# Kernel optimization log

Hardware: AMD Instinct MI355X
Metric: run time of the kernel (lower is better)

Reference implementation:

```python
import jax, jax.numpy as jnp
import numpy as np

N, M, D = 16384, 4096, 512
GAMMA = 1.0


def setup_inputs() -> dict:
    key = jax.random.key(0)
    kx, kc = jax.random.split(key)
    x = jax.random.normal(kx, (N, D), dtype=jnp.float32)
    centroids = jax.random.normal(kc, (M, D), dtype=jnp.float32)
    return {"x": x, "centroids": centroids}


def reference(x, centroids):
    x_sq = jnp.sum(x * x, axis=-1, keepdims=True)            # [N, 1]
    c_sq = jnp.sum(centroids * centroids, axis=-1)           # [M]
    cross = jnp.einsum('nd,md->nm', x, centroids)            # [N, M]
    dist_sq = x_sq + c_sq[None, :] - 2.0 * cross
    dist_sq = jnp.maximum(dist_sq, 0.0)  # clamp tiny negatives from fp error
    return jnp.exp(-GAMMA * dist_sq)
```

## Files before the change

kernel.cpp:

```cpp
#include <hip/hip_runtime.h>
#include <hip/hip_bf16.h>


#define NN 16384
#define MM 4096
#define DD 512

typedef float f32x4 __attribute__((ext_vector_type(4)));
typedef long i64x2 __attribute__((ext_vector_type(2)));

__device__ __forceinline__ void async16(const void* g, void* l) {
  __builtin_amdgcn_global_load_lds(
      (const __attribute__((address_space(1))) void*)g,
      (__attribute__((address_space(3))) void*)l, 16, 0, 0);
}

#define MFMA8(a, b, c) __builtin_amdgcn_mfma_f32_16x16x32_fp8_fp8(a, b, c, 0, 0, 0)
#define WAITVM(n) asm volatile("s_waitcnt vmcnt(" #n ")" ::: "memory")
#define GLD4(dst, addr) \
  asm volatile("global_load_dwordx4 %0, %1, off" : "=v"(dst) : "v"(addr))
#define GLD1(dst, addr) \
  asm volatile("global_load_dword %0, %1, off" : "=v"(dst) : "v"(addr))

__global__ __launch_bounds__(256) void prep_fp8(
    const float* __restrict__ x, const float* __restrict__ c,
    unsigned char* __restrict__ x8, unsigned char* __restrict__ c8,
    float* __restrict__ xsq, float* __restrict__ csq) {
  const int w = threadIdx.x >> 6;
  const int lane = threadIdx.x & 63;
  int row = blockIdx.x * 4 + w;
  const float* src = x;
  unsigned char* dst = x8;
  float* sq = xsq;
  if (row >= NN) {
    row -= NN;
    src = c; dst = c8; sq = csq;
    if (row >= MM) return;
  }
  const float* p = src + (size_t)row * DD + lane * 8;
  float4 v0 = *(const float4*)p;
  float4 v1 = *(const float4*)(p + 4);
  float vv[8] = {v0.x, v0.y, v0.z, v0.w, v1.x, v1.y, v1.z, v1.w};
  float s = 0.f;
#pragma unroll
  for (int j = 0; j < 8; ++j) s += vv[j] * vv[j];
  int pk0 = __builtin_amdgcn_cvt_pk_fp8_f32(vv[0], vv[1], 0, false);
  int pk1 = __builtin_amdgcn_cvt_pk_fp8_f32(vv[2], vv[3], 0, false);
  int pk2 = __builtin_amdgcn_cvt_pk_fp8_f32(vv[4], vv[5], 0, false);
  int pk3 = __builtin_amdgcn_cvt_pk_fp8_f32(vv[6], vv[7], 0, false);
  uint2 wrd;
  wrd.x = (unsigned)(pk0 & 0xFFFF) | ((unsigned)pk1 << 16);
  wrd.y = (unsigned)(pk2 & 0xFFFF) | ((unsigned)pk3 << 16);
  const int db = ((lane >> 3) << 6) + ((lane & 3) << 4) + (((lane >> 2) & 1) << 3);
  *(uint2*)(dst + (size_t)row * DD + db) = wrd;
#pragma unroll
  for (int o = 32; o >= 1; o >>= 1) s += __shfl_down(s, o);
  if (lane == 0) sq[row] = s;
}

__global__ __launch_bounds__(512, 2) void rbf_gemm(
    const unsigned char* __restrict__ x8, const unsigned char* __restrict__ c8,
    const float* __restrict__ xsq, const float* __restrict__ csq,
    float* __restrict__ out) {
  __shared__ __attribute__((aligned(16))) unsigned char smem[49152];

  const int t = threadIdx.x;
  const int w = t >> 6;
  const int lane = t & 63;
  const int fr = lane & 15;
  const int fq = lane >> 4;
  const int wr = w >> 2;
  const int wc = w & 3;

  const int bid = blockIdx.x;
  const int a = bid & 7, qq = bid >> 3;
  const int x0 = ((a << 4) + (qq >> 2)) << 7;
  const int strip = qq & 3;

  const int srow = t >> 2;
  const int ssl = ((t & 3) ^ ((t >> 3) & 3)) << 4;
  const unsigned char* gx = x8 + (size_t)(x0 + srow) * DD + ssl;
  const unsigned char* gc = c8 + (size_t)srow * DD + ssl;

#define COFF(v, i)                                                        \
  ((size_t)(((((strip) << 2) + ((v) >> 3)) << 8) + (i) * 128) * DD +      \
   ((v) & 7) * 64)

  const int sxor = (fq ^ ((fr >> 1) & 3)) << 4;
  const int rcb = (wc * 64 + fr) * 64 + sxor;
  const int rxb = (wr * 64 + fr) * 64 + sxor;

  f32x4 aA[4][4], aB[4][4];
  f32x4 csA[4], csB[4];
  float xsr[4];

#define STFRAG(AO, CS, CPRE, S)                                               \
  do {                                                                        \
    f32x4 _v;                                                                 \
    _Pragma("unroll") for (int _j = 0; _j < 4; ++_j) {                        \
      float _t = __builtin_fmaf(                                              \
          AO[(S) >> 2][(S)&3][_j], 2.8853900817779268f,                       \
          __builtin_fmaf(CS[(S)&3][_j], -1.4426950408889634f,                 \
                         xsr[(S) >> 2] * -1.4426950408889634f));              \
      _v[_j] = fminf(__builtin_exp2f(_t), 1.0f);                              \
    }                                                                         \
    *(f32x4*)(out + (size_t)(x0 + wr * 64 + (((S) >> 2) << 4) + fr) * MM +    \
              (CPRE) + wc * 64 + (((S)&3) << 4) + (fq << 2)) = _v;            \
  } while (0)

#define MF4(AN, Q, V)                                                     \
  do {                                                                    \
    _Pragma("unroll") for (int _n = 0; _n < 4; ++_n) {                    \
      f32x4 _c = ((V)&7) == 0 ? (f32x4){0.f, 0.f, 0.f, 0.f} : AN[Q][_n];  \
      _c = MFMA8(cf[_n][0], xq[0], _c);                                   \
      AN[Q][_n] = MFMA8(cf[_n][1], xq[1], _c);                            \
    }                                                                     \
  } while (0)

#define KT(V, AN, AO, CS, SEN, CPRE, CSLD, CSB, CSOT, VMN)                    \
  do {                                                                        \
    const char* bX = (const char*)smem + (((V)&1) << 13);                     \
    const char* bC = (const char*)smem + 16384 + (((V)&1) << 14);             \
    char* dXw = (char*)smem + ((((V) + 1) & 1) << 13) + (w << 10);            \
    char* dCw = (char*)smem + 16384 + (((V)&1) << 14) + (w << 10);            \
    i64x2 cf[4], xq;                                                          \
    cf[0] = *(const i64x2*)(bC + rcb);                                        \
    cf[1] = *(const i64x2*)(bC + rcb + 1024);                                 \
    cf[2] = *(const i64x2*)(bC + rcb + 2048);                                 \
    cf[3] = *(const i64x2*)(bC + rcb + 3072);                                 \
    xq = *(const i64x2*)(bX + rxb);                                           \
    if ((V) + 1 < 32) async16(gx + (((V) + 1) & 7) * 64, dXw);                \
    if (CSLD) {                                                               \
      const float* _cp =                                                      \
          csq + (((strip << 2) + (CSOT)) << 8) + wc * 64 + (fq << 2);         \
      GLD4(CSB[0], _cp);                                                      \
      GLD4(CSB[1], _cp + 16);                                                 \
      GLD4(CSB[2], _cp + 32);                                                 \
      GLD4(CSB[3], _cp + 48);                                                 \
    }                                                                         \
    __builtin_amdgcn_s_barrier();                                             \
    asm volatile("s_waitcnt lgkmcnt(0)" ::: "memory");                        \
    __builtin_amdgcn_s_setprio(1);                                            \
    MF4(AN, 0, V);                                                            \
    __builtin_amdgcn_s_setprio(0);                                            \
    __builtin_amdgcn_s_barrier();                                             \
    xq = *(const i64x2*)(bX + rxb + 1024);                                    \
    if ((V) + 2 < 32) async16(gc + COFF((V) + 2, 0), dCw);                    \
    if (SEN) STFRAG(AO, CS, CPRE, 2 * ((V)&7));                               \
    __builtin_amdgcn_s_barrier();                                             \
    asm volatile("s_waitcnt lgkmcnt(0)" ::: "memory");                        \
    __builtin_amdgcn_s_setprio(1);                                            \
    MF4(AN, 1, V);                                                            \
    __builtin_amdgcn_s_setprio(0);                                            \
    __builtin_amdgcn_s_barrier();                                             \
    xq = *(const i64x2*)(bX + rxb + 2048);                                    \
    if ((V) + 2 < 32) async16(gc + COFF((V) + 2, 1), dCw + 8192);             \
    __builtin_amdgcn_s_barrier();                                             \
    asm volatile("s_waitcnt lgkmcnt(0)" ::: "memory");                        \
    __builtin_amdgcn_s_setprio(1);                                            \
    MF4(AN, 2, V);                                                            \
    __builtin_amdgcn_s_setprio(0);                                            \
    __builtin_amdgcn_s_barrier();                                             \
    xq = *(const i64x2*)(bX + rxb + 3072);                                    \
    if (SEN) STFRAG(AO, CS, CPRE, 2 * ((V)&7) + 1);                           \
    __builtin_amdgcn_s_barrier();                                             \
    asm volatile("s_waitcnt lgkmcnt(0)" ::: "memory");                        \
    __builtin_amdgcn_s_setprio(1);                                            \
    MF4(AN, 3, V);                                                            \
    __builtin_amdgcn_s_setprio(0);                                            \
    WAITVM(VMN);                                                              \
    __builtin_amdgcn_s_barrier();                                             \
    __builtin_amdgcn_sched_barrier(0);                                        \
  } while (0)

  const int CP0 = ((strip << 2) + 0) << 8;
  const int CP1 = ((strip << 2) + 1) << 8;
  const int CP2 = ((strip << 2) + 2) << 8;
  const int CP3 = ((strip << 2) + 3) << 8;

  {
    const float* cp = csq + (CP0 + wc * 64 + (fq << 2));
    GLD4(csA[0], cp); GLD4(csA[1], cp + 16);
    GLD4(csA[2], cp + 32); GLD4(csA[3], cp + 48);
    const float* xp = xsq + x0 + wr * 64 + fr;
    GLD1(xsr[0], xp); GLD1(xsr[1], xp + 16);
    GLD1(xsr[2], xp + 32); GLD1(xsr[3], xp + 48);
  }
  async16(gc + COFF(0, 0), (char*)smem + 16384 + (w << 10));
  async16(gc + COFF(0, 1), (char*)smem + 16384 + 8192 + (w << 10));
  async16(gx, (char*)smem + (w << 10));
  async16(gc + COFF(1, 0), (char*)smem + 32768 + (w << 10));
  async16(gc + COFF(1, 1), (char*)smem + 32768 + 8192 + (w << 10));
  WAITVM(2);
  __builtin_amdgcn_s_barrier();
  __builtin_amdgcn_sched_barrier(0);

  KT(0, aA, aB, csA, 0, CP0, 0, csB, 0, 2);
  KT(1, aA, aB, csA, 0, CP0, 0, csB, 0, 2);
  KT(2, aA, aB, csA, 0, CP0, 0, csB, 0, 2);
  KT(3, aA, aB, csA, 0, CP0, 0, csB, 0, 2);
  KT(4, aA, aB, csA, 0, CP0, 0, csB, 0, 2);
  KT(5, aA, aB, csA, 0, CP0, 0, csB, 0, 2);
  KT(6, aA, aB, csA, 0, CP0, 0, csB, 0, 2);
  KT(7, aA, aB, csA, 0, CP0, 0, csB, 0, 2);
  KT(8, aB, aA, csA, 1, CP0, 0, csB, 1, 4);
  KT(9, aB, aA, csA, 1, CP0, 0, csB, 1, 4);
  KT(10, aB, aA, csA, 1, CP0, 0, csB, 1, 4);
  KT(11, aB, aA, csA, 1, CP0, 0, csB, 1, 4);
  KT(12, aB, aA, csA, 1, CP0, 0, csB, 1, 4);
  KT(13, aB, aA, csA, 1, CP0, 0, csB, 1, 4);
  KT(14, aB, aA, csA, 1, CP0, 1, csB, 1, 8);
  KT(15, aB, aA, csA, 1, CP0, 0, csB, 1, 4);
  KT(16, aA, aB, csB, 1, CP1, 0, csA, 2, 4);
  KT(17, aA, aB, csB, 1, CP1, 0, csA, 2, 4);
  KT(18, aA, aB, csB, 1, CP1, 0, csA, 2, 4);
  KT(19, aA, aB, csB, 1, CP1, 0, csA, 2, 4);
  KT(20, aA, aB, csB, 1, CP1, 0, csA, 2, 4);
  KT(21, aA, aB, csB, 1, CP1, 0, csA, 2, 4);
  KT(22, aA, aB, csB, 1, CP1, 1, csA, 2, 8);
  KT(23, aA, aB, csB, 1, CP1, 0, csA, 2, 4);
  KT(24, aB, aA, csA, 1, CP2, 0, csB, 3, 4);
  KT(25, aB, aA, csA, 1, CP2, 0, csB, 3, 4);
  KT(26, aB, aA, csA, 1, CP2, 0, csB, 3, 4);
  KT(27, aB, aA, csA, 1, CP2, 0, csB, 3, 4);
  KT(28, aB, aA, csA, 1, CP2, 0, csB, 3, 4);
  KT(29, aB, aA, csA, 1, CP2, 0, csB, 3, 4);
  KT(30, aB, aA, csA, 1, CP2, 1, csB, 3, 6);
  KT(31, aB, aA, csA, 1, CP2, 0, csB, 3, 4);

#pragma unroll
  for (int S = 0; S < 16; ++S) STFRAG(aB, csB, CP3, S);
}

__global__ void rbf_naive(const float* __restrict__ x,
                          const float* __restrict__ c,
                          float* __restrict__ out) {
  __shared__ float sx[16][17], sc[16][17];
  const int tx = threadIdx.x, ty = threadIdx.y;
  const int row = blockIdx.y * 16 + ty;
  const int colb = blockIdx.x * 16;
  float d = 0.f;
  for (int k0 = 0; k0 < DD; k0 += 16) {
    sx[ty][tx] = x[(size_t)row * DD + k0 + tx];
    sc[ty][tx] = c[(size_t)(colb + ty) * DD + k0 + tx];
    __syncthreads();
#pragma unroll
    for (int k = 0; k < 16; ++k) {
      float diff = sx[ty][k] - sc[tx][k];
      d += diff * diff;
    }
    __syncthreads();
  }
  out[(size_t)row * MM + colb + tx] = __expf(-d);
}

extern "C" void kernel_launch(void* const* d_in, const int* in_sizes, int n_in,
                              void* d_out, int out_size, void* d_ws,
                              size_t ws_size, hipStream_t stream) {
  const float* x = (const float*)d_in[0];
  const float* c = (const float*)d_in[1];
  float* out = (float*)d_out;

  char* ws = (char*)d_ws;
  unsigned char* x8 = (unsigned char*)ws;
  unsigned char* c8 = x8 + (size_t)NN * DD;
  float* xsq = (float*)(c8 + (size_t)MM * DD);
  float* csq = xsq + NN;
  const size_t need = (size_t)((char*)(csq + MM) - ws);

  if (ws_size < need) {
    dim3 grid(MM / 16, NN / 16), block(16, 16);
    rbf_naive<<<grid, block, 0, stream>>>(x, c, out);
    return;
  }

  prep_fp8<<<(NN + MM) / 4, 256, 0, stream>>>(x, c, x8, c8, xsq, csq);
  rbf_gemm<<<512, 512, 0, stream>>>(x8, c8, xsq, csq, out);
}
```

Measured before the change: 99.59 us.

## Transpose accumulator tiles through LDS so each wave stores full contiguous output rows

The epilogue no longer writes MFMA fragments straight to global memory in 16-byte pieces scattered across rows. Accumulator fragments are staged through a new swizzled 32 KB LDS region, and each wave reads back whole 1024-column rows. It then applies the exp and writes lane-contiguous 16-byte stores that cover a full 4 KB row segment, so global stores coalesce better. The cost is a larger shared memory footprint (80 KB per block, which may limit occupancy under launch_bounds(512,2)), extra LDS traffic and barriers, and a reworked csq/xsq load schedule and vmcnt wait counts.

```diff
diff --git a/kernel.cpp b/kernel.cpp
--- a/kernel.cpp
+++ b/kernel.cpp
@@ -17,10 +17,10 @@
 
 #define MFMA8(a, b, c) __builtin_amdgcn_mfma_f32_16x16x32_fp8_fp8(a, b, c, 0, 0, 0)
 #define WAITVM(n) asm volatile("s_waitcnt vmcnt(" #n ")" ::: "memory")
+#define LGKM0 asm volatile("s_waitcnt lgkmcnt(0)" ::: "memory")
+#define BAR __builtin_amdgcn_s_barrier()
 #define GLD4(dst, addr) \
   asm volatile("global_load_dwordx4 %0, %1, off" : "=v"(dst) : "v"(addr))
-#define GLD1(dst, addr) \
-  asm volatile("global_load_dword %0, %1, off" : "=v"(dst) : "v"(addr))
 
 __global__ __launch_bounds__(256) void prep_fp8(
     const float* __restrict__ x, const float* __restrict__ c,
@@ -62,7 +62,7 @@
     const unsigned char* __restrict__ x8, const unsigned char* __restrict__ c8,
     const float* __restrict__ xsq, const float* __restrict__ csq,
     float* __restrict__ out) {
-  __shared__ __attribute__((aligned(16))) unsigned char smem[49152];
+  __shared__ __attribute__((aligned(16))) unsigned char smem[81920];
 
   const int t = threadIdx.x;
   const int w = t >> 6;
@@ -82,8 +82,8 @@
   const unsigned char* gx = x8 + (size_t)(x0 + srow) * DD + ssl;
   const unsigned char* gc = c8 + (size_t)srow * DD + ssl;
 
-#define COFF(v, i)                                                        \
-  ((size_t)(((((strip) << 2) + ((v) >> 3)) << 8) + (i) * 128) * DD +      \
+#define COFF(v, i)                                                   \
+  ((size_t)(((((strip) << 2) + ((v) >> 3)) << 8) + (i) * 128) * DD + \
    ((v) & 7) * 64)
 
   const int sxor = (fq ^ ((fr >> 1) & 3)) << 4;
@@ -91,86 +91,94 @@
   const int rxb = (wr * 64 + fr) * 64 + sxor;
 
   f32x4 aA[4][4], aB[4][4];
-  f32x4 csA[4], csB[4];
-  float xsr[4];
-
-#define STFRAG(AO, CS, CPRE, S)                                               \
+  f32x4 csTX, csTY, xsE[4];
+
+#define MF4(AN, Q, V)                                                    \
+  do {                                                                   \
+    _Pragma("unroll") for (int _n = 0; _n < 4; ++_n) {                   \
+      f32x4 _c = ((V)&7) == 0 ? (f32x4){0.f, 0.f, 0.f, 0.f} : AN[Q][_n]; \
+      _c = MFMA8(cf[_n][0], xq[0], _c);                                  \
+      AN[Q][_n] = MFMA8(cf[_n][1], xq[1], _c);                           \
+    }                                                                    \
+  } while (0)
+
+#define TWRITE(AO, CH)                                                     \
+  do {                                                                     \
+    _Pragma("unroll") for (int _ms = 0; _ms < 2; ++_ms) {                  \
+      const int _rl = _ms * 16 + fr;                                       \
+      _Pragma("unroll") for (int _n = 0; _n < 4; ++_n) {                   \
+        const int _g = (wc << 4) + (_n << 2) + fq;                         \
+        *(f32x4*)((char*)smem + 49152 + _rl * 1024 +                       \
+                  (((_g + _rl) & 63) << 4)) = AO[2 * ((CH)&1) + _ms][_n];  \
+      }                                                                    \
+    }                                                                      \
+  } while (0)
+
+#define TREAD(CH)                                                          \
+  t0 = *(const f32x4*)((char*)smem + 49152 + ((w << 2) + 0) * 1024 +       \
+                       (((lane + (w << 2) + 0) & 63) << 4));               \
+  t1 = *(const f32x4*)((char*)smem + 49152 + ((w << 2) + 1) * 1024 +       \
+                       (((lane + (w << 2) + 1) & 63) << 4));               \
+  t2 = *(const f32x4*)((char*)smem + 49152 + ((w << 2) + 2) * 1024 +       \
+                       (((lane + (w << 2) + 2) & 63) << 4));               \
+  t3 = *(const f32x4*)((char*)smem + 49152 + ((w << 2) + 3) * 1024 +       \
+                       (((lane + (w << 2) + 3) & 63) << 4));
+
+#define EXPST1(TV, CH, RI, CSU, CPREO)                                        \
   do {                                                                        \
+    const float _xn = xsE[CH][RI] * -1.4426950408889634f;                     \
     f32x4 _v;                                                                 \
     _Pragma("unroll") for (int _j = 0; _j < 4; ++_j) {                        \
-      float _t = __builtin_fmaf(                                              \
-          AO[(S) >> 2][(S)&3][_j], 2.8853900817779268f,                       \
-          __builtin_fmaf(CS[(S)&3][_j], -1.4426950408889634f,                 \
-                         xsr[(S) >> 2] * -1.4426950408889634f));              \
-      _v[_j] = fminf(__builtin_exp2f(_t), 1.0f);                              \
+      float _arg = __builtin_fmaf(                                            \
+          TV[_j], 2.8853900817779268f,                                        \
+          __builtin_fmaf(CSU[_j], -1.4426950408889634f, _xn));                \
+      _v[_j] = fminf(__builtin_exp2f(_arg), 1.0f);                            \
     }                                                                         \
-    *(f32x4*)(out + (size_t)(x0 + wr * 64 + (((S) >> 2) << 4) + fr) * MM +    \
-              (CPRE) + wc * 64 + (((S)&3) << 4) + (fq << 2)) = _v;            \
-  } while (0)
-
-#define MF4(AN, Q, V)                                                     \
-  do {                                                                    \
-    _Pragma("unroll") for (int _n = 0; _n < 4; ++_n) {                    \
-      f32x4 _c = ((V)&7) == 0 ? (f32x4){0.f, 0.f, 0.f, 0.f} : AN[Q][_n];  \
-      _c = MFMA8(cf[_n][0], xq[0], _c);                                   \
-      AN[Q][_n] = MFMA8(cf[_n][1], xq[1], _c);                            \
-    }                                                                     \
-  } while (0)
-
-#define KT(V, AN, AO, CS, SEN, CPRE, CSLD, CSB, CSOT, VMN)                    \
+    *(f32x4*)(out + (size_t)(x0 + (CH)*32 + (w << 2) + (RI)) * MM + (CPREO) + \
+              (lane << 2)) = _v;                                              \
+  } while (0)
+
+#define EXPST4(CH, CSU, CPREO) \
+  EXPST1(t0, CH, 0, CSU, CPREO); EXPST1(t1, CH, 1, CSU, CPREO); \
+  EXPST1(t2, CH, 2, CSU, CPREO); EXPST1(t3, CH, 3, CSU, CPREO);
+
+#define KT(V, AN, AO, EACT, CPREO, CSU, CSLD, CSL, CSOT, DOVM, VMN)           \
   do {                                                                        \
     const char* bX = (const char*)smem + (((V)&1) << 13);                     \
     const char* bC = (const char*)smem + 16384 + (((V)&1) << 14);             \
     char* dXw = (char*)smem + ((((V) + 1) & 1) << 13) + (w << 10);            \
     char* dCw = (char*)smem + 16384 + (((V)&1) << 14) + (w << 10);            \
     i64x2 cf[4], xq;                                                          \
+    f32x4 t0, t1, t2, t3;                                                     \
     cf[0] = *(const i64x2*)(bC + rcb);                                        \
     cf[1] = *(const i64x2*)(bC + rcb + 1024);                                 \
     cf[2] = *(const i64x2*)(bC + rcb + 2048);                                 \
     cf[3] = *(const i64x2*)(bC + rcb + 3072);                                 \
     xq = *(const i64x2*)(bX + rxb);                                           \
+    if (CSLD)                                                                 \
+      GLD4(CSL, csq + ((((strip) << 2) + (CSOT)) << 8) + (lane << 2));        \
     if ((V) + 1 < 32) async16(gx + (((V) + 1) & 7) * 64, dXw);                \
-    if (CSLD) {                                                               \
-      const float* _cp =                                                      \
-          csq + (((strip << 2) + (CSOT)) << 8) + wc * 64 + (fq << 2);         \
-      GLD4(CSB[0], _cp);                                                      \
-      GLD4(CSB[1], _cp + 16);                                                 \
-      GLD4(CSB[2], _cp + 32);                                                 \
-      GLD4(CSB[3], _cp + 48);                                                 \
-    }                                                                         \
-    __builtin_amdgcn_s_barrier();                                             \
-    asm volatile("s_waitcnt lgkmcnt(0)" ::: "memory");                        \
-    __builtin_amdgcn_s_setprio(1);                                            \
-    MF4(AN, 0, V);                                                            \
-    __builtin_amdgcn_s_setprio(0);                                            \
-    __builtin_amdgcn_s_barrier();                                             \
+    BAR; LGKM0;                                                               \
+    __builtin_amdgcn_s_setprio(1); MF4(AN, 0, V); __builtin_amdgcn_s_setprio(0); \
+    BAR;                                                                      \
     xq = *(const i64x2*)(bX + rxb + 1024);                                    \
     if ((V) + 2 < 32) async16(gc + COFF((V) + 2, 0), dCw);                    \
-    if (SEN) STFRAG(AO, CS, CPRE, 2 * ((V)&7));                               \
-    __builtin_amdgcn_s_barrier();                                             \
-    asm volatile("s_waitcnt lgkmcnt(0)" ::: "memory");                        \
-    __builtin_amdgcn_s_setprio(1);                                            \
-    MF4(AN, 1, V);                                                            \
-    __builtin_amdgcn_s_setprio(0);                                            \
-    __builtin_amdgcn_s_barrier();                                             \
+    if ((EACT) && ((V)&1)) { TREAD(((V)&7) >> 1); }                           \
+    BAR; LGKM0;                                                               \
+    __builtin_amdgcn_s_setprio(1); MF4(AN, 1, V); __builtin_amdgcn_s_setprio(0); \
+    if ((EACT) && ((V)&1)) { EXPST4(((V)&7) >> 1, CSU, CPREO); }              \
+    BAR;                                                                      \
     xq = *(const i64x2*)(bX + rxb + 2048);                                    \
     if ((V) + 2 < 32) async16(gc + COFF((V) + 2, 1), dCw + 8192);             \
-    __builtin_amdgcn_s_barrier();                                             \
-    asm volatile("s_waitcnt lgkmcnt(0)" ::: "memory");                        \
-    __builtin_amdgcn_s_setprio(1);                                            \
-    MF4(AN, 2, V);                                                            \
-    __builtin_amdgcn_s_setprio(0);                                            \
-    __builtin_amdgcn_s_barrier();                                             \
+    BAR; LGKM0;                                                               \
+    __builtin_amdgcn_s_setprio(1); MF4(AN, 2, V); __builtin_amdgcn_s_setprio(0); \
+    if ((EACT) && !((V)&1) && wr == (((V)&7) >> 2)) { TWRITE(AO, ((V)&7) >> 1); } \
+    BAR;                                                                      \
     xq = *(const i64x2*)(bX + rxb + 3072);                                    \
-    if (SEN) STFRAG(AO, CS, CPRE, 2 * ((V)&7) + 1);                           \
-    __builtin_amdgcn_s_barrier();                                             \
-    asm volatile("s_waitcnt lgkmcnt(0)" ::: "memory");                        \
-    __builtin_amdgcn_s_setprio(1);                                            \
-    MF4(AN, 3, V);                                                            \
-    __builtin_amdgcn_s_setprio(0);                                            \
-    WAITVM(VMN);                                                              \
-    __builtin_amdgcn_s_barrier();                                             \
-    __builtin_amdgcn_sched_barrier(0);                                        \
+    BAR; LGKM0;                                                               \
+    __builtin_amdgcn_s_setprio(1); MF4(AN, 3, V); __builtin_amdgcn_s_setprio(0); \
+    if (DOVM) WAITVM(VMN);                                                    \
+    BAR; __builtin_amdgcn_sched_barrier(0);                                   \
   } while (0)
 
   const int CP0 = ((strip << 2) + 0) << 8;
@@ -179,12 +187,9 @@
   const int CP3 = ((strip << 2) + 3) << 8;
 
   {
-    const float* cp = csq + (CP0 + wc * 64 + (fq << 2));
-    GLD4(csA[0], cp); GLD4(csA[1], cp + 16);
-    GLD4(csA[2], cp + 32); GLD4(csA[3], cp + 48);
-    const float* xp = xsq + x0 + wr * 64 + fr;
-    GLD1(xsr[0], xp); GLD1(xsr[1], xp + 16);
-    GLD1(xsr[2], xp + 32); GLD1(xsr[3], xp + 48);
+    const float* xp = xsq + x0 + (w << 2);
+    GLD4(xsE[0], xp); GLD4(xsE[1], xp + 32);
+    GLD4(xsE[2], xp + 64); GLD4(xsE[3], xp + 96);
   }
   async16(gc + COFF(0, 0), (char*)smem + 16384 + (w << 10));
   async16(gc + COFF(0, 1), (char*)smem + 16384 + 8192 + (w << 10));
@@ -192,44 +197,55 @@
   async16(gc + COFF(1, 0), (char*)smem + 32768 + (w << 10));
   async16(gc + COFF(1, 1), (char*)smem + 32768 + 8192 + (w << 10));
   WAITVM(2);
-  __builtin_amdgcn_s_barrier();
+  BAR;
   __builtin_amdgcn_sched_barrier(0);
 
-  KT(0, aA, aB, csA, 0, CP0, 0, csB, 0, 2);
-  KT(1, aA, aB, csA, 0, CP0, 0, csB, 0, 2);
-  KT(2, aA, aB, csA, 0, CP0, 0, csB, 0, 2);
-  KT(3, aA, aB, csA, 0, CP0, 0, csB, 0, 2);
-  KT(4, aA, aB, csA, 0, CP0, 0, csB, 0, 2);
-  KT(5, aA, aB, csA, 0, CP0, 0, csB, 0, 2);
-  KT(6, aA, aB, csA, 0, CP0, 0, csB, 0, 2);
-  KT(7, aA, aB, csA, 0, CP0, 0, csB, 0, 2);
-  KT(8, aB, aA, csA, 1, CP0, 0, csB, 1, 4);
-  KT(9, aB, aA, csA, 1, CP0, 0, csB, 1, 4);
-  KT(10, aB, aA, csA, 1, CP0, 0, csB, 1, 4);
-  KT(11, aB, aA, csA, 1, CP0, 0, csB, 1, 4);
-  KT(12, aB, aA, csA, 1, CP0, 0, csB, 1, 4);
-  KT(13, aB, aA, csA, 1, CP0, 0, csB, 1, 4);
-  KT(14, aB, aA, csA, 1, CP0, 1, csB, 1, 8);
-  KT(15, aB, aA, csA, 1, CP0, 0, csB, 1, 4);
-  KT(16, aA, aB, csB, 1, CP1, 0, csA, 2, 4);
-  KT(17, aA, aB, csB, 1, CP1, 0, csA, 2, 4);
-  KT(18, aA, aB, csB, 1, CP1, 0, csA, 2, 4);
-  KT(19, aA, aB, csB, 1, CP1, 0, csA, 2, 4);
-  KT(20, aA, aB, csB, 1, CP1, 0, csA, 2, 4);
-  KT(21, aA, aB, csB, 1, CP1, 0, csA, 2, 4);
-  KT(22, aA, aB, csB, 1, CP1, 1, csA, 2, 8);
-  KT(23, aA, aB, csB, 1, CP1, 0, csA, 2, 4);
-  KT(24, aB, aA, csA, 1, CP2, 0, csB, 3, 4);
-  KT(25, aB, aA, csA, 1, CP2, 0, csB, 3, 4);
-  KT(26, aB, aA, csA, 1, CP2, 0, csB, 3, 4);
-  KT(27, aB, aA, csA, 1, CP2, 0, csB, 3, 4);
-  KT(28, aB, aA, csA, 1, CP2, 0, csB, 3, 4);
-  KT(29, aB, aA, csA, 1, CP2, 0, csB, 3, 4);
-  KT(30, aB, aA, csA, 1, CP2, 1, csB, 3, 6);
-  KT(31, aB, aA, csA, 1, CP2, 0, csB, 3, 4);
-
-#pragma unroll
-  for (int S = 0; S < 16; ++S) STFRAG(aB, csB, CP3, S);
+  KT(0, aA, aB, 0, CP0, csTX, 0, csTX, 0, 1, 2);
+  KT(1, aA, aB, 0, CP0, csTX, 0, csTX, 0, 1, 2);
+  KT(2, aA, aB, 0, CP0, csTX, 0, csTX, 0, 1, 2);
+  KT(3, aA, aB, 0, CP0, csTX, 0, csTX, 0, 1, 2);
+  KT(4, aA, aB, 0, CP0, csTX, 0, csTX, 0, 1, 2);
+  KT(5, aA, aB, 0, CP0, csTX, 0, csTX, 0, 1, 2);
+  KT(6, aA, aB, 0, CP0, csTX, 1, csTX, 0, 1, 2);
+  KT(7, aA, aB, 0, CP0, csTX, 0, csTX, 0, 1, 2);
+  KT(8, aB, aA, 1, CP0, csTX, 0, csTY, 1, 1, 2);
+  KT(9, aB, aA, 1, CP0, csTX, 0, csTY, 1, 1, 6);
+  KT(10, aB, aA, 1, CP0, csTX, 0, csTY, 1, 1, 2);
+  KT(11, aB, aA, 1, CP0, csTX, 0, csTY, 1, 1, 6);
+  KT(12, aB, aA, 1, CP0, csTX, 0, csTY, 1, 1, 2);
+  KT(13, aB, aA, 1, CP0, csTX, 0, csTY, 1, 1, 6);
+  KT(14, aB, aA, 1, CP0, csTX, 1, csTY, 1, 1, 2);
+  KT(15, aB, aA, 1, CP0, csTX, 0, csTY, 1, 1, 6);
+  KT(16, aA, aB, 1, CP1, csTY, 0, csTX, 2, 1, 2);
+  KT(17, aA, aB, 1, CP1, csTY, 0, csTX, 2, 1, 6);
+  KT(18, aA, aB, 1, CP1, csTY, 0, csTX, 2, 1, 2);
+  KT(19, aA, aB, 1, CP1, csTY, 0, csTX, 2, 1, 6);
+  KT(20, aA, aB, 1, CP1, csTY, 0, csTX, 2, 1, 2);
+  KT(21, aA, aB, 1, CP1, csTY, 0, csTX, 2, 1, 6);
+  KT(22, aA, aB, 1, CP1, csTY, 1, csTX, 2, 1, 2);
+  KT(23, aA, aB, 1, CP1, csTY, 0, csTX, 2, 1, 6);
+  KT(24, aB, aA, 1, CP2, csTX, 0, csTY, 3, 1, 2);
+  KT(25, aB, aA, 1, CP2, csTX, 0, csTY, 3, 1, 6);
+  KT(26, aB, aA, 1, CP2, csTX, 0, csTY, 3, 1, 2);
+  KT(27, aB, aA, 1, CP2, csTX, 0, csTY, 3, 1, 6);
+  KT(28, aB, aA, 1, CP2, csTX, 0, csTY, 3, 1, 2);
+  KT(29, aB, aA, 1, CP2, csTX, 0, csTY, 3, 1, 6);
+  KT(30, aB, aA, 1, CP2, csTX, 1, csTY, 3, 1, 0);
+  KT(31, aB, aA, 1, CP2, csTX, 0, csTY, 3, 0, 0);
+
+#define TAILC(CH)                                                  \
+  do {                                                             \
+    BAR;                                                           \
+    if (wr == ((CH) >> 1)) { TWRITE(aB, CH); }                     \
+    LGKM0;                                                         \
+    BAR;                                                           \
+    f32x4 t0, t1, t2, t3;                                          \
+    TREAD(CH);                                                     \
+    LGKM0;                                                         \
+    EXPST4(CH, csTY, CP3);                                         \
+  } while (0)
+  TAILC(0); TAILC(1); TAILC(2); TAILC(3);
+#undef TAILC
 }
 
 __global__ void rbf_naive(const float* __restrict__ x,
```

Result: slower. 106.0 us (+6.4%).

## Halve barriers per k-tile and batch epilogue stores into 4-fragment groups

Applied to the files above, without the earlier changes.

Restructures the pipelined FP8 MFMA k-tile step: each step now loads two X fragments at once and issues two MFMA groups per phase, so the barriers per tile drop from six to two. The epilogue for the previous tile is emitted as one 4x4 fragment group on every other k-tile instead of two single fragments per tile. The centroid-norm loads are rescheduled and use renamed ping-pong register sets. The aim is to cut barrier stalls and let more MFMAs issue back to back. The cost is higher register pressure from the extra X fragment, and the changed vmcnt accounting may be wrong.

```diff
diff --git a/kernel.cpp b/kernel.cpp
--- a/kernel.cpp
+++ b/kernel.cpp
@@ -17,6 +17,8 @@
 
 #define MFMA8(a, b, c) __builtin_amdgcn_mfma_f32_16x16x32_fp8_fp8(a, b, c, 0, 0, 0)
 #define WAITVM(n) asm volatile("s_waitcnt vmcnt(" #n ")" ::: "memory")
+#define LGKM0 asm volatile("s_waitcnt lgkmcnt(0)" ::: "memory")
+#define BAR __builtin_amdgcn_s_barrier()
 #define GLD4(dst, addr) \
   asm volatile("global_load_dwordx4 %0, %1, off" : "=v"(dst) : "v"(addr))
 #define GLD1(dst, addr) \
@@ -82,8 +84,8 @@
   const unsigned char* gx = x8 + (size_t)(x0 + srow) * DD + ssl;
   const unsigned char* gc = c8 + (size_t)srow * DD + ssl;
 
-#define COFF(v, i)                                                        \
-  ((size_t)(((((strip) << 2) + ((v) >> 3)) << 8) + (i) * 128) * DD +      \
+#define COFF(v, i)                                                   \
+  ((size_t)(((((strip) << 2) + ((v) >> 3)) << 8) + (i) * 128) * DD + \
    ((v) & 7) * 64)
 
   const int sxor = (fq ^ ((fr >> 1) & 3)) << 4;
@@ -91,86 +93,75 @@
   const int rxb = (wr * 64 + fr) * 64 + sxor;
 
   f32x4 aA[4][4], aB[4][4];
-  f32x4 csA[4], csB[4];
+  f32x4 csX[4], csY[4];
   float xsr[4];
 
-#define STFRAG(AO, CS, CPRE, S)                                               \
-  do {                                                                        \
-    f32x4 _v;                                                                 \
-    _Pragma("unroll") for (int _j = 0; _j < 4; ++_j) {                        \
-      float _t = __builtin_fmaf(                                              \
-          AO[(S) >> 2][(S)&3][_j], 2.8853900817779268f,                       \
-          __builtin_fmaf(CS[(S)&3][_j], -1.4426950408889634f,                 \
-                         xsr[(S) >> 2] * -1.4426950408889634f));              \
-      _v[_j] = fminf(__builtin_exp2f(_t), 1.0f);                              \
-    }                                                                         \
-    *(f32x4*)(out + (size_t)(x0 + wr * 64 + (((S) >> 2) << 4) + fr) * MM +    \
-              (CPRE) + wc * 64 + (((S)&3) << 4) + (fq << 2)) = _v;            \
+#define MF4(AN, Q, XQ, V)                                                \
+  do {                                                                   \
+    _Pragma("unroll") for (int _n = 0; _n < 4; ++_n) {                   \
+      f32x4 _c = ((V)&7) == 0 ? (f32x4){0.f, 0.f, 0.f, 0.f} : AN[Q][_n]; \
+      _c = MFMA8(cf[_n][0], XQ[0], _c);                                  \
+      AN[Q][_n] = MFMA8(cf[_n][1], XQ[1], _c);                           \
+    }                                                                    \
   } while (0)
 
-#define MF4(AN, Q, V)                                                     \
-  do {                                                                    \
-    _Pragma("unroll") for (int _n = 0; _n < 4; ++_n) {                    \
-      f32x4 _c = ((V)&7) == 0 ? (f32x4){0.f, 0.f, 0.f, 0.f} : AN[Q][_n];  \
-      _c = MFMA8(cf[_n][0], xq[0], _c);                                   \
-      AN[Q][_n] = MFMA8(cf[_n][1], xq[1], _c);                            \
-    }                                                                     \
+#define STFRAG4(AO, M, CSU, CPREO)                                          \
+  do {                                                                      \
+    const float _xn = xsr[M] * -1.4426950408889634f;                        \
+    float* _orow =                                                          \
+        out + (size_t)(x0 + wr * 64 + (M)*16 + fr) * MM + (CPREO) +         \
+        wc * 64 + (fq << 2);                                                \
+    _Pragma("unroll") for (int _n = 0; _n < 4; ++_n) {                      \
+      f32x4 _v;                                                             \
+      _Pragma("unroll") for (int _j = 0; _j < 4; ++_j) {                    \
+        float _arg = __builtin_fmaf(                                        \
+            AO[M][_n][_j], 2.8853900817779268f,                             \
+            __builtin_fmaf(CSU[_n][_j], -1.4426950408889634f, _xn));        \
+        _v[_j] = fminf(__builtin_exp2f(_arg), 1.0f);                        \
+      }                                                                     \
+      *(f32x4*)(_orow + _n * 16) = _v;                                      \
+    }                                                                       \
   } while (0)
 
-#define KT(V, AN, AO, CS, SEN, CPRE, CSLD, CSB, CSOT, VMN)                    \
-  do {                                                                        \
-    const char* bX = (const char*)smem + (((V)&1) << 13);                     \
-    const char* bC = (const char*)smem + 16384 + (((V)&1) << 14);             \
-    char* dXw = (char*)smem + ((((V) + 1) & 1) << 13) + (w << 10);            \
-    char* dCw = (char*)smem + 16384 + (((V)&1) << 14) + (w << 10);            \
-    i64x2 cf[4], xq;                                                          \
-    cf[0] = *(const i64x2*)(bC + rcb);                                        \
-    cf[1] = *(const i64x2*)(bC + rcb + 1024);                                 \
-    cf[2] = *(const i64x2*)(bC + rcb + 2048);                                 \
-    cf[3] = *(const i64x2*)(bC + rcb + 3072);                                 \
-    xq = *(const i64x2*)(bX + rxb);                                           \
-    if ((V) + 1 < 32) async16(gx + (((V) + 1) & 7) * 64, dXw);                \
-    if (CSLD) {                                                               \
-      const float* _cp =                                                      \
-          csq + (((strip << 2) + (CSOT)) << 8) + wc * 64 + (fq << 2);         \
-      GLD4(CSB[0], _cp);                                                      \
-      GLD4(CSB[1], _cp + 16);                                                 \
-      GLD4(CSB[2], _cp + 32);                                                 \
-      GLD4(CSB[3], _cp + 48);                                                 \
-    }                                                                         \
-    __builtin_amdgcn_s_barrier();                                             \
-    asm volatile("s_waitcnt lgkmcnt(0)" ::: "memory");                        \
-    __builtin_amdgcn_s_setprio(1);                                            \
-    MF4(AN, 0, V);                                                            \
-    __builtin_amdgcn_s_setprio(0);                                            \
-    __builtin_amdgcn_s_barrier();                                             \
-    xq = *(const i64x2*)(bX + rxb + 1024);                                    \
-    if ((V) + 2 < 32) async16(gc + COFF((V) + 2, 0), dCw);                    \
-    if (SEN) STFRAG(AO, CS, CPRE, 2 * ((V)&7));                               \
-    __builtin_amdgcn_s_barrier();                                             \
-    asm volatile("s_waitcnt lgkmcnt(0)" ::: "memory");                        \
-    __builtin_amdgcn_s_setprio(1);                                            \
-    MF4(AN, 1, V);                                                            \
-    __builtin_amdgcn_s_setprio(0);                                            \
-    __builtin_amdgcn_s_barrier();                                             \
-    xq = *(const i64x2*)(bX + rxb + 2048);                                    \
-    if ((V) + 2 < 32) async16(gc + COFF((V) + 2, 1), dCw + 8192);             \
-    __builtin_amdgcn_s_barrier();                                             \
-    asm volatile("s_waitcnt lgkmcnt(0)" ::: "memory");                        \
-    __builtin_amdgcn_s_setprio(1);                                            \
-    MF4(AN, 2, V);                                                            \
-    __builtin_amdgcn_s_setprio(0);                                            \
-    __builtin_amdgcn_s_barrier();                                             \
-    xq = *(const i64x2*)(bX + rxb + 3072);                                    \
-    if (SEN) STFRAG(AO, CS, CPRE, 2 * ((V)&7) + 1);                           \
-    __builtin_amdgcn_s_barrier();                                             \
-    asm volatile("s_waitcnt lgkmcnt(0)" ::: "memory");                        \
-    __builtin_amdgcn_s_setprio(1);                                            \
-    MF4(AN, 3, V);                                                            \
-    __builtin_amdgcn_s_setprio(0);                                            \
-    WAITVM(VMN);                                                              \
-    __builtin_amdgcn_s_barrier();                                             \
-    __builtin_amdgcn_sched_barrier(0);                                        \
+#define KT(V, AN, AO, SEN, CPREO, CSU, CSLD, CSL, CSOT, DOVM, VMN)            \
+  do {                                                                       \
+    const char* bX = (const char*)smem + (((V)&1) << 13);                    \
+    const char* bC = (const char*)smem + 16384 + (((V)&1) << 14);            \
+    char* dXw = (char*)smem + ((((V) + 1) & 1) << 13) + (w << 10);           \
+    char* dCw = (char*)smem + 16384 + (((V)&1) << 14) + (w << 10);           \
+    i64x2 cf[4], xqA, xqB;                                                   \
+    cf[0] = *(const i64x2*)(bC + rcb);                                       \
+    cf[1] = *(const i64x2*)(bC + rcb + 1024);                                \
+    cf[2] = *(const i64x2*)(bC + rcb + 2048);                                \
+    cf[3] = *(const i64x2*)(bC + rcb + 3072);                                \
+    xqA = *(const i64x2*)(bX + rxb);                                         \
+    xqB = *(const i64x2*)(bX + rxb + 1024);                                  \
+    if (CSLD) {                                                              \
+      const float* _cp =                                                     \
+          csq + ((((strip) << 2) + (CSOT)) << 8) + wc * 64 + (fq << 2);      \
+      GLD4(CSL[0], _cp); GLD4(CSL[1], _cp + 16);                             \
+      GLD4(CSL[2], _cp + 32); GLD4(CSL[3], _cp + 48);                        \
+    }                                                                        \
+    if ((V) + 1 < 32) async16(gx + (((V) + 1) & 7) * 64, dXw);               \
+    LGKM0;                                                                   \
+    __builtin_amdgcn_s_setprio(1);                                           \
+    MF4(AN, 0, xqA, V);                                                      \
+    MF4(AN, 1, xqB, V);                                                      \
+    __builtin_amdgcn_s_setprio(0);                                           \
+    BAR;     \
+    xqA = *(const i64x2*)(bX + rxb + 2048);                                  \
+    xqB = *(const i64x2*)(bX + rxb + 3072);                                  \
+    if ((V) + 2 < 32) async16(gc + COFF((V) + 2, 0), dCw);                   \
+    if (SEN) STFRAG4(AO, ((V)&7) >> 1, CSU, CPREO);                          \
+    if ((V) + 2 < 32) async16(gc + COFF((V) + 2, 1), dCw + 8192);            \
+    LGKM0;                                                                   \
+    __builtin_amdgcn_s_setprio(1);                                           \
+    MF4(AN, 2, xqA, V);                                                      \
+    MF4(AN, 3, xqB, V);                                                      \
+    __builtin_amdgcn_s_setprio(0);                                           \
+    if (DOVM) WAITVM(VMN);                                                   \
+    BAR;                                                                     \
+    __builtin_amdgcn_sched_barrier(0);                                       \
   } while (0)
 
   const int CP0 = ((strip << 2) + 0) << 8;
@@ -179,9 +170,6 @@
   const int CP3 = ((strip << 2) + 3) << 8;
 
   {
-    const float* cp = csq + (CP0 + wc * 64 + (fq << 2));
-    GLD4(csA[0], cp); GLD4(csA[1], cp + 16);
-    GLD4(csA[2], cp + 32); GLD4(csA[3], cp + 48);
     const float* xp = xsq + x0 + wr * 64 + fr;
     GLD1(xsr[0], xp); GLD1(xsr[1], xp + 16);
     GLD1(xsr[2], xp + 32); GLD1(xsr[3], xp + 48);
@@ -192,44 +180,46 @@
   async16(gc + COFF(1, 0), (char*)smem + 32768 + (w << 10));
   async16(gc + COFF(1, 1), (char*)smem + 32768 + 8192 + (w << 10));
   WAITVM(2);
-  __builtin_amdgcn_s_barrier();
+  BAR;
   __builtin_amdgcn_sched_barrier(0);
 
-  KT(0, aA, aB, csA, 0, CP0, 0, csB, 0, 2);
-  KT(1, aA, aB, csA, 0, CP0, 0, csB, 0, 2);
-  KT(2, aA, aB, csA, 0, CP0, 0, csB, 0, 2);
-  KT(3, aA, aB, csA, 0, CP0, 0, csB, 0, 2);
-  KT(4, aA, aB, csA, 0, CP0, 0, csB, 0, 2);
-  KT(5, aA, aB, csA, 0, CP0, 0, csB, 0, 2);
-  KT(6, aA, aB, csA, 0, CP0, 0, csB, 0, 2);
-  KT(7, aA, aB, csA, 0, CP0, 0, csB, 0, 2);
-  KT(8, aB, aA, csA, 1, CP0, 0, csB, 1, 4);
-  KT(9, aB, aA, csA, 1, CP0, 0, csB, 1, 4);
-  KT(10, aB, aA, csA, 1, CP0, 0, csB, 1, 4);
-  KT(11, aB, aA, csA, 1, CP0, 0, csB, 1, 4);
-  KT(12, aB, aA, csA, 1, CP0, 0, csB, 1, 4);
-  KT(13, aB, aA, csA, 1, CP0, 0, csB, 1, 4);
-  KT(14, aB, aA, csA, 1, CP0, 1, csB, 1, 8);
-  KT(15, aB, aA, csA, 1, CP0, 0, csB, 1, 4);
-  KT(16, aA, aB, csB, 1, CP1, 0, csA, 2, 4);
-  KT(17, aA, aB, csB, 1, CP1, 0, csA, 2, 4);
-  KT(18, aA, aB, csB, 1, CP1, 0, csA, 2, 4);
-  KT(19, aA, aB, csB, 1, CP1, 0, csA, 2, 4);
-  KT(20, aA, aB, csB, 1, CP1, 0, csA, 2, 4);
-  KT(21, aA, aB, csB, 1, CP1, 0, csA, 2, 4);
-  KT(22, aA, aB, csB, 1, CP1, 1, csA, 2, 8);
-  KT(23, aA, aB, csB, 1, CP1, 0, csA, 2, 4);
-  KT(24, aB, aA, csA, 1, CP2, 0, csB, 3, 4);
-  KT(25, aB, aA, csA, 1, CP2, 0, csB, 3, 4);
-  KT(26, aB, aA, csA, 1, CP2, 0, csB, 3, 4);
-  KT(27, aB, aA, csA, 1, CP2, 0, csB, 3, 4);
-  KT(28, aB, aA, csA, 1, CP2, 0, csB, 3, 4);
-  KT(29, aB, aA, csA, 1, CP2, 0, csB, 3, 4);
-  KT(30, aB, aA, csA, 1, CP2, 1, csB, 3, 6);
-  KT(31, aB, aA, csA, 1, CP2, 0, csB, 3, 4);
-
-#pragma unroll
-  for (int S = 0; S < 16; ++S) STFRAG(aB, csB, CP3, S);
+  KT(0, aA, aB, 0, CP0, csX, 0, csX, 0, 1, 2);
+  KT(1, aA, aB, 0, CP0, csX, 0, csX, 0, 1, 2);
+  KT(2, aA, aB, 0, CP0, csX, 0, csX, 0, 1, 2);
+  KT(3, aA, aB, 0, CP0, csX, 0, csX, 0, 1, 2);
+  KT(4, aA, aB, 0, CP0, csX, 0, csX, 0, 1, 2);
+  KT(5, aA, aB, 0, CP0, csX, 0, csX, 0, 1, 2);
+  KT(6, aA, aB, 0, CP0, csX, 1, csX, 0, 1, 2);
+  KT(7, aA, aB, 0, CP0, csX, 0, csX, 0, 1, 2);
+  KT(8, aB, aA, 0, CP0, csX, 0, csY, 1, 1, 2);
+  KT(9, aB, aA, 1, CP0, csX, 0, csY, 1, 1, 6);
+  KT(10, aB, aA, 0, CP0, csX, 0, csY, 1, 1, 2);
+  KT(11, aB, aA, 1, CP0, csX, 0, csY, 1, 1, 6);
+  KT(12, aB, aA, 0, CP0, csX, 0, csY, 1, 1, 2);
+  KT(13, aB, aA, 1, CP0, csX, 0, csY, 1, 1, 6);
+  KT(14, aB, aA, 0, CP0, csX, 1, csY, 1, 1, 2);
+  KT(15, aB, aA, 1, CP0, csX, 0, csY, 1, 1, 6);
+  KT(16, aA, aB, 0, CP1, csY, 0, csX, 2, 1, 2);
+  KT(17, aA, aB, 1, CP1, csY, 0, csX, 2, 1, 6);
+  KT(18, aA, aB, 0, CP1, csY, 0, csX, 2, 1, 2);
+  KT(19, aA, aB, 1, CP1, csY, 0, csX, 2, 1, 6);
+  KT(20, aA, aB, 0, CP1, csY, 0, csX, 2, 1, 2);
+  KT(21, aA, aB, 1, CP1, csY, 0, csX, 2, 1, 6);
+  KT(22, aA, aB, 0, CP1, csY, 1, csX, 2, 1, 2);
+  KT(23, aA, aB, 1, CP1, csY, 0, csX, 2, 1, 6);
+  KT(24, aB, aA, 0, CP2, csX, 0, csY, 3, 1, 2);
+  KT(25, aB, aA, 1, CP2, csX, 0, csY, 3, 1, 6);
+  KT(26, aB, aA, 0, CP2, csX, 0, csY, 3, 1, 2);
+  KT(27, aB, aA, 1, CP2, csX, 0, csY, 3, 1, 6);
+  KT(28, aB, aA, 0, CP2, csX, 0, csY, 3, 1, 2);
+  KT(29, aB, aA, 1, CP2, csX, 0, csY, 3, 1, 6);
+  KT(30, aB, aA, 0, CP2, csX, 1, csY, 3, 1, 0);
+  KT(31, aB, aA, 1, CP2, csX, 0, csY, 3, 0, 0);
+
+  STFRAG4(aB, 0, csY, CP3);
+  STFRAG4(aB, 1, csY, CP3);
+  STFRAG4(aB, 2, csY, CP3);
+  STFRAG4(aB, 3, csY, CP3);
 }
 
 __global__ void rbf_naive(const float* __restrict__ x,
```

Measured after the change: 101.6 us. Within noise of the previous version (+2.0%).
